# Optimization experiments

Hardware: AMD Instinct MI355X
Metric: run time of the kernel (lower is better)

Reference implementation:

```python
import jax, jax.numpy as jnp
import numpy as np

B, K, D, H = 4, 2048, 1024, 16
NCTX = K // 2
IMAGE_SIZE = 224
MAX_POS = 1024


def _build_rope_cache_2d(max_pos, dim, base=10000.0):
    half_dim = dim // 2
    theta = 1.0 / base ** (np.arange(0, half_dim, 2, dtype=np.float32) / half_dim)
    positions = np.arange(max_pos, dtype=np.float32)
    freqs = np.outer(positions, theta)  # [max_pos, dim/4]
    return jnp.asarray(np.stack([np.cos(freqs), np.sin(freqs)], axis=-1))  # [max_pos, dim/4, 2]


def apply_rope_2d(x, coords, rope_cache, image_size):
    b, k, d = x.shape
    half, quarter = d // 2, d // 4
    max_pos = rope_cache.shape[0]
    cn = jnp.clip(coords / image_size * (max_pos - 1), 0, max_pos - 1)
    y_pos = cn[..., 0].astype(jnp.int32)
    x_pos = cn[..., 1].astype(jnp.int32)
    y_rope = rope_cache[y_pos]  # [b,k,quarter,2]
    x_rope = rope_cache[x_pos]

    def rot(part, r):
        c, s = r[..., 0], r[..., 1]
        p0, p1 = part[..., 0], part[..., 1]
        return jnp.stack([p0 * c - p1 * s, p0 * s + p1 * c], -1).reshape(b, k, half)

    xp = x[..., :half].reshape(b, k, quarter, 2)
    yp = x[..., half:].reshape(b, k, quarter, 2)
    return jnp.concatenate([rot(xp, x_rope), rot(yp, y_rope)], -1)


def mha(q_tok, kv_tok, in_w, in_b, out_w, out_b, num_heads):
    b, nq, d = q_tok.shape
    hd = d // num_heads
    wq, wk, wv = jnp.split(in_w, 3, axis=0)
    bq, bk, bv = jnp.split(in_b, 3)
    q = (q_tok @ wq.T + bq).reshape(b, nq, num_heads, hd)
    k = (kv_tok @ wk.T + bk).reshape(b, -1, num_heads, hd)
    v = (kv_tok @ wv.T + bv).reshape(b, -1, num_heads, hd)
    s = jnp.einsum('bqhd,bkhd->bhqk', q, k) / jnp.sqrt(jnp.asarray(hd, q.dtype))
    a = jax.nn.softmax(s, axis=-1)
    o = jnp.einsum('bhqk,bkhd->bqhd', a, v).reshape(b, nq, d)
    return o @ out_w.T + out_b


def setup_inputs() -> dict:
    key = jax.random.key(0)
    ks = jax.random.split(key, 12)
    sc = 1.0 / np.sqrt(D)
    x = jax.random.normal(ks[0], (B, K, D), jnp.float32)
    coords = jax.random.uniform(ks[1], (B, K, 2), jnp.float32) * IMAGE_SIZE
    # boolean context mask with exactly NCTX context tokens per batch (code assumes equal counts)
    perms = jax.vmap(lambda k_: jax.random.permutation(k_, K))(jax.random.split(ks[2], B))
    is_context = jax.vmap(lambda m, i: m.at[i].set(True))(jnp.zeros((B, K), bool), perms[:, :NCTX])
    rope_cache = _build_rope_cache_2d(MAX_POS, D)
    return {
        'x': x, 'coords': coords, 'is_context': is_context, 'rope_cache': rope_cache,
        'ctx_in_w': jax.random.normal(ks[3], (3 * D, D), jnp.float32) * sc,
        'ctx_in_b': jnp.zeros((3 * D,), jnp.float32),
        'ctx_out_w': jax.random.normal(ks[4], (D, D), jnp.float32) * sc,
        'ctx_out_b': jnp.zeros((D,), jnp.float32),
        'tgt_in_w': jax.random.normal(ks[5], (3 * D, D), jnp.float32) * sc,
        'tgt_in_b': jnp.zeros((3 * D,), jnp.float32),
        'tgt_out_w': jax.random.normal(ks[6], (D, D), jnp.float32) * sc,
        'tgt_out_b': jnp.zeros((D,), jnp.float32),
    }


def reference(x, coords, is_context, rope_cache,
              ctx_in_w, ctx_in_b, ctx_out_w, ctx_out_b,
              tgt_in_w, tgt_in_b, tgt_out_w, tgt_out_b):
    # 2D RoPE before attention (as in the backbone)
    xr = apply_rope_2d(x, coords, rope_cache, IMAGE_SIZE)
    # stable argsort: context positions (key 0) first, in original order
    order = jnp.argsort(jnp.where(is_context, 0, 1), axis=1, stable=True)
    ctx_idx = order[:, :NCTX]   # [B, NCTX]
    tgt_idx = order[:, NCTX:]   # [B, K-NCTX]
    ctx_tok = jnp.take_along_axis(xr, ctx_idx[..., None], axis=1)
    tgt_tok = jnp.take_along_axis(xr, tgt_idx[..., None], axis=1)
    ctx_out = mha(ctx_tok, ctx_tok, ctx_in_w, ctx_in_b, ctx_out_w, ctx_out_b, H)
    tgt_out = mha(tgt_tok, ctx_tok, tgt_in_w, tgt_in_b, tgt_out_w, tgt_out_b, H)
    out = jnp.zeros_like(x)
    out = jax.vmap(lambda o, i, v: o.at[i].set(v))(out, ctx_idx, ctx_out)
    out = jax.vmap(lambda o, i, v: o.at[i].set(v))(out, tgt_idx, tgt_out)
    return out
```

## Files before the change

### kernel.cpp

```cpp
#include <hip/hip_runtime.h>
#include <math.h>

#define B_    4
#define K_    2048
#define D_    1024
#define H_    16
#define NCTX_ 1024

typedef unsigned short ushort_t;
typedef _Float16 f16;
typedef __attribute__((ext_vector_type(8))) _Float16 f16x8;
typedef __attribute__((ext_vector_type(4))) float f32x4;

union U4 {
  f16 h[4];
  ushort4 u;
};

union P4 {
  f16 h[4];
  ushort4 u;
};

__device__ __forceinline__ void gload16(const void* g, void* l) {
  __builtin_amdgcn_global_load_lds(
      (const __attribute__((address_space(1))) unsigned int*)g,
      (__attribute__((address_space(3))) unsigned int*)l, 16, 0, 0);
}

__global__ __launch_bounds__(256) void partition_kernel(
    const unsigned char* __restrict__ isctx, int* __restrict__ pos,
    int* __restrict__ ipos) {
  const int b = blockIdx.x;
  const int tid = threadIdx.x;
  const int wid = tid >> 6, lane = tid & 63;
  __shared__ int csum[4];
  __shared__ int waveTot[4];
  __shared__ int strideSh;

  int cnt = 0;
  for (int i = 0; i < 32; ++i) cnt += (isctx[tid * 32 + i] != 0);
  for (int off = 32; off; off >>= 1) cnt += __shfl_down(cnt, off, 64);
  if (lane == 0) csum[wid] = cnt;
  __syncthreads();
  if (tid == 0) {
    int t = csum[0] + csum[1] + csum[2] + csum[3];
    strideSh = (t > 2048) ? 1 : ((t > 768) ? 4 : 8);
  }
  __syncthreads();
  const int stride = strideSh;

  const unsigned char* base = isctx + (size_t)b * K_ * stride;
  int f[8];
  int s = 0;
  for (int i = 0; i < 8; ++i) {
    f[i] = base[(size_t)(tid * 8 + i) * stride] != 0;
    s += f[i];
  }
  int inc = s;
  for (int off = 1; off < 64; off <<= 1) {
    int v = __shfl_up(inc, off, 64);
    if (lane >= off) inc += v;
  }
  if (lane == 63) waveTot[wid] = inc;
  __syncthreads();
  int wOff = 0;
  for (int w = 0; w < wid; ++w) wOff += waveTot[w];
  int run = wOff + inc - s;
  for (int i = 0; i < 8; ++i) {
    int k = tid * 8 + i;
    int p;
    if (f[i]) {
      p = run;
      run++;
    } else {
      p = NCTX_ + k - run;
    }
    pos[b * K_ + k] = p;
    ipos[b * K_ + p] = k;
  }
}

__global__ __launch_bounds__(256) void rope_kernel(
    const float* __restrict__ x, const float* __restrict__ coords,
    const float* __restrict__ cache, const int* __restrict__ ipos,
    f16* __restrict__ tok) {
  const int row = blockIdx.x;
  const int b = row >> 11;
  const int r = row & (K_ - 1);
  const int k = ipos[row];
  const int t = threadIdx.x;

  const float cy = coords[(size_t)(b * K_ + k) * 2 + 0];
  const float cx = coords[(size_t)(b * K_ + k) * 2 + 1];
  const int ypos = (int)fminf(fmaxf(cy / 224.0f * 1023.0f, 0.0f), 1023.0f);
  const int xpos = (int)fminf(fmaxf(cx / 224.0f * 1023.0f, 0.0f), 1023.0f);

  const float4 v = ((const float4*)(x + ((size_t)b * K_ + k) * D_))[t];
  const int e = 4 * t;
  const float* crow;
  int coff;
  if (e < 512) {
    crow = cache + (size_t)xpos * 512;
    coff = e;
  } else {
    crow = cache + (size_t)ypos * 512;
    coff = e - 512;
  }
  const float4 cs = *(const float4*)(crow + coff);
  float o[4];
  o[0] = v.x * cs.x - v.y * cs.y;
  o[1] = v.x * cs.y + v.y * cs.x;
  o[2] = v.z * cs.z - v.w * cs.w;
  o[3] = v.z * cs.w + v.w * cs.z;
  U4 h;
#pragma unroll
  for (int i = 0; i < 4; ++i) h.h[i] = (f16)o[i];
  ((ushort4*)(tok + ((size_t)b * K_ + r) * D_))[t] = h.u;
}

__global__ __launch_bounds__(256) void cvt_all(
    const float* __restrict__ ctx_in_w, const float* __restrict__ tgt_in_w,
    const float* __restrict__ ctx_out_w, const float* __restrict__ tgt_out_w,
    f16* __restrict__ dst) {
  const int i4 = blockIdx.x * 256 + threadIdx.x;
  const int f = i4 * 4;
  const float* src;
  if (f < 3145728) src = ctx_in_w + f;
  else if (f < 5242880) src = tgt_in_w + (f - 3145728 + 1048576);
  else if (f < 6291456) src = tgt_in_w + (f - 5242880);
  else if (f < 7340032) src = ctx_out_w + (f - 6291456);
  else src = tgt_out_w + (f - 7340032);
  const float4 v = *(const float4*)src;
  U4 u;
  u.h[0] = (f16)v.x;
  u.h[1] = (f16)v.y;
  u.h[2] = (f16)v.z;
  u.h[3] = (f16)v.w;
  ((ushort4*)dst)[i4] = u.u;
}

#define GEMM_PRE(AP, WP, Kd)                                                  \
  const int rb_ = wave * 8 + (lane >> 3);          \
  const int kk_ = ((lane & 7) ^ (lane >> 3)) * 8;   \
  const f16* gA_ = (AP) + (size_t)rb_ * (Kd) + kk_;                           \
  const f16* gW_ = (WP) + (size_t)rb_ * (Kd) + kk_;                           \
  const int lA_ = wave * 8 * 64 + lane * 8;

#define GEMM_STAGE(k0s, bb)                                                   \
  _Pragma("unroll") for (int j = 0; j < 4; ++j) {                             \
    gload16(gA_ + (size_t)j * 32 * Kd_ + (k0s), &lds[(bb) + j * 2048 + lA_]); \
    gload16(gW_ + (size_t)j * 32 * Kd_ + (k0s),                               \
            &lds[(bb) + 8192 + j * 2048 + lA_]);                              \
  }

#define GEMM_TILE(bb)                                                         \
  _Pragma("unroll") for (int kh = 0; kh < 2; ++kh) {                          \
    f16x8 af[4], wf[4];                                                       \
    _Pragma("unroll") for (int i = 0; i < 4; ++i) {                           \
      const int ca = ((kh * 4 + quad) ^ (m16 & 7)) * 8;                       \
      af[i] = *(const f16x8*)&lds[(bb) + (wm + i * 16 + m16) * 64 + ca];      \
      wf[i] =                                                                 \
          *(const f16x8*)&lds[(bb) + 8192 + (wn + i * 16 + m16) * 64 + ca];   \
    }                                                                         \
    _Pragma("unroll") for (int i = 0; i < 4; ++i)                             \
        _Pragma("unroll") for (int j = 0; j < 4; ++j)                         \
      acc[i][j] = __builtin_amdgcn_mfma_f32_16x16x32_f16(af[i], wf[j],        \
                                                         acc[i][j], 0, 0, 0); \
  }

#define GEMM_CORE(AP, WP, Kd)                                                 \
  f32x4 acc[4][4];                                                            \
  {                                                                           \
    const f32x4 z = {0.f, 0.f, 0.f, 0.f};                                     \
    for (int i = 0; i < 4; ++i)                                               \
      for (int j = 0; j < 4; ++j) acc[i][j] = z;                              \
  }                                                                           \
  const int Kd_ = (Kd);                                                       \
  GEMM_PRE(AP, WP, Kd_)                                                       \
  GEMM_STAGE(0, 0)                                                            \
  for (int t = 0; t < Kd_ / 64; ++t) {                                        \
    const int cb = (t & 1) * 16384;                                           \
    if (t + 1 < Kd_ / 64) {                                                   \
      GEMM_STAGE((t + 1) * 64, ((t + 1) & 1) * 16384)                         \
      asm volatile("s_waitcnt vmcnt(8)" ::: "memory");                        \
    } else {                                                                  \
      asm volatile("s_waitcnt vmcnt(0)" ::: "memory");                        \
    }                                                                         \
    __builtin_amdgcn_s_barrier();                                             \
    asm volatile("" ::: "memory");                                            \
    GEMM_TILE(cb)                                                             \
    asm volatile("" ::: "memory");                                            \
    __builtin_amdgcn_s_barrier();                                             \
  }

__global__ __launch_bounds__(256, 2) void gemm_proj(
    const f16* __restrict__ tok, const f16* __restrict__ wcat,
    const float* __restrict__ ctx_in_b, const float* __restrict__ tgt_in_b,
    f16* __restrict__ qkvc, f16* __restrict__ kvt, f16* __restrict__ qt) {
  __shared__ f16 lds[32768];
  const int tid = threadIdx.x;
  const int wave = tid >> 6, lane = tid & 63;
  const int quad = lane >> 4, m16 = lane & 15;
  const int nb = blockIdx.x, mb = blockIdx.y, b = blockIdx.z;
  const int wm = (wave & 1) << 6, wn = (wave >> 1) << 6;
  const int m0 = mb * 128;
  const bool isQ = nb >= 40;
  const int n0 = isQ ? (nb - 40) * 128 : nb * 128;
  const f16* AP = tok + (size_t)b * K_ * D_ +
                  (isQ ? (size_t)NCTX_ * D_ : (size_t)0) + (size_t)m0 * D_;
  const f16* WP = wcat + (isQ ? (size_t)5242880 : (size_t)0) +
                  (size_t)n0 * D_;

  GEMM_CORE(AP, WP, D_)

#pragma unroll
  for (int j = 0; j < 4; ++j) {
    const int col = n0 + wn + j * 16 + m16;
    float bv;
    f16* dst;
    int ldc, dcol;
    if (isQ) {
      bv = tgt_in_b[col];
      dst = qt + (size_t)b * NCTX_ * D_;
      ldc = D_;
      dcol = col;
    } else if (col < 3072) {
      bv = ctx_in_b[col];
      dst = qkvc + (size_t)b * NCTX_ * 3072;
      ldc = 3072;
      dcol = col;
    } else {
      bv = tgt_in_b[D_ + col - 3072];
      dst = kvt + (size_t)b * NCTX_ * 2048;
      ldc = 2048;
      dcol = col - 3072;
    }
#pragma unroll
    for (int i = 0; i < 4; ++i) {
      const int mr = m0 + wm + i * 16 + quad * 4;
#pragma unroll
      for (int r = 0; r < 4; ++r)
        dst[(size_t)(mr + r) * ldc + dcol] = (f16)(acc[i][j][r] + bv);
    }
  }
}

__global__ __launch_bounds__(256, 2) void gemm_out(
    const f16* __restrict__ Atok, const f16* __restrict__ Wbase,
    const float* __restrict__ bias_ctx, const float* __restrict__ bias_tgt,
    const int* __restrict__ ipos, float* __restrict__ out) {
  __shared__ f16 lds[32768];
  const int tid = threadIdx.x;
  const int wave = tid >> 6, lane = tid & 63;
  const int quad = lane >> 4, m16 = lane & 15;
  const int n0 = blockIdx.x * 128, m0 = blockIdx.y * 128;
  const int b = blockIdx.z & 3, sel = blockIdx.z >> 2;
  const int wm = (wave & 1) << 6, wn = (wave >> 1) << 6;
  const f16* AP = Atok + (size_t)b * K_ * D_ + (size_t)sel * NCTX_ * D_ +
                  (size_t)m0 * D_;
  const f16* WP = Wbase + (size_t)sel * 1048576 + (size_t)n0 * D_;
  const float* bias = sel ? bias_tgt : bias_ctx;

  GEMM_CORE(AP, WP, D_)

#pragma unroll
  for (int j = 0; j < 4; ++j) {
    const int col = n0 + wn + j * 16 + m16;
    const float bv = bias[col];
#pragma unroll
    for (int i = 0; i < 4; ++i) {
      const int mr = m0 + wm + i * 16 + quad * 4;
#pragma unroll
      for (int r = 0; r < 4; ++r) {
        const int orow = ipos[b * K_ + sel * NCTX_ + mr + r];
        out[(size_t)b * K_ * D_ + (size_t)orow * D_ + col] =
            acc[i][j][r] + bv;
      }
    }
  }
}

__global__ __launch_bounds__(256) void vtrans_kernel(
    const ushort_t* __restrict__ V, long long sVb, int ldv, int coloff,
    ushort_t* __restrict__ Vt) {
  __shared__ __align__(16) ushort_t tile[64][72];
  const int tblk = blockIdx.x, h = blockIdx.y, b = blockIdx.z;
  const int tid = threadIdx.x;
  const ushort_t* src =
      V + (long long)b * sVb + (size_t)(tblk * 64) * ldv + coloff + h * 64;
#pragma unroll
  for (int j = 0; j < 2; ++j) {
    const int c = j * 256 + tid;
    const int r = c >> 3, dc = c & 7;
    *(uint4*)&tile[r][dc * 8] = *(const uint4*)(src + (size_t)r * ldv + dc * 8);
  }
  __syncthreads();
  ushort_t* dst = Vt + (size_t)(b * H_ + h) * 64 * 1024 + tblk * 64;
#pragma unroll
  for (int j = 0; j < 2; ++j) {
    const int c = j * 256 + tid;
    const int d = c >> 3, tc = c & 7;
    union {
      ushort_t u[8];
      uint4 v;
    } t;
#pragma unroll
    for (int i = 0; i < 8; ++i) t.u[i] = tile[tc * 8 + i][d];
    *(uint4*)(dst + (size_t)d * 1024 + tc * 8) = t.v;
  }
}

__global__ __launch_bounds__(512) void attn_mfma(
    const f16* __restrict__ Qp, long long sQb, int ldq,
    const f16* __restrict__ Kp, long long sKb, int ldk,
    const f16* __restrict__ Vt, f16* __restrict__ O, long long sOb) {
  __shared__ f16 QP[8192];
  __shared__ f16 Ks[2][4096];
  __shared__ f16 Vs[2][4096];
  const int tid = threadIdx.x, wave = tid >> 6, lane = tid & 63;
  const int quad = lane >> 4, m16 = lane & 15;
  const int q0 = blockIdx.x * 128, h = blockIdx.y, b = blockIdx.z;
  const f16* Qb = Qp + (long long)b * sQb + h * 64;
  const f16* Kb = Kp + (long long)b * sKb + h * 64;
  const f16* Vb = Vt + (size_t)(b * H_ + h) * 64 * 1024;

  const int rowS = tid >> 3;
  const int kkc = ((tid & 7) ^ (rowS & 7)) * 8;
  const int lB = tid * 8;

#pragma unroll
  for (int j = 0; j < 2; ++j)
    gload16(Qb + (size_t)(q0 + j * 64 + rowS) * ldq + kkc,
            &QP[j * 4096 + lB]);
  gload16(Kb + (size_t)rowS * ldk + kkc, &Ks[0][lB]);
  gload16(Vb + (size_t)rowS * 1024 + kkc, &Vs[0][lB]);

  float m_run = -1e30f, l_run = 0.f;
  f32x4 Oa[4];
  const f32x4 z = {0.f, 0.f, 0.f, 0.f};
#pragma unroll
  for (int j = 0; j < 4; ++j) Oa[j] = z;

  asm volatile("s_waitcnt vmcnt(2)" ::: "memory");
  __builtin_amdgcn_s_barrier();

  const int c0 = (quad ^ (m16 & 7)) * 8;
  const int c1 = ((quad + 4) ^ (m16 & 7)) * 8;
  const f16x8 qf0 = *(const f16x8*)&QP[(wave * 16 + m16) * 64 + c0];
  const f16x8 qf1 = *(const f16x8*)&QP[(wave * 16 + m16) * 64 + c1];

  f16* Pw = QP + wave * 1024;

  for (int kt = 0; kt < 16; ++kt) {
    const int cur = kt & 1;
    if (kt < 15) {
      gload16(Kb + (size_t)((kt + 1) * 64 + rowS) * ldk + kkc,
              &Ks[cur ^ 1][lB]);
      gload16(Vb + (size_t)rowS * 1024 + (kt + 1) * 64 + kkc,
              &Vs[cur ^ 1][lB]);
      asm volatile("s_waitcnt vmcnt(2)" ::: "memory");
    } else {
      asm volatile("s_waitcnt vmcnt(0)" ::: "memory");
    }
    __builtin_amdgcn_s_barrier();

    f32x4 S[4];
    __builtin_amdgcn_s_setprio(1);
#pragma unroll
    for (int jn = 0; jn < 4; ++jn) {
      S[jn] = z;
      const f16x8 kf0 = *(const f16x8*)&Ks[cur][(jn * 16 + m16) * 64 + c0];
      const f16x8 kf1 = *(const f16x8*)&Ks[cur][(jn * 16 + m16) * 64 + c1];
      S[jn] = __builtin_amdgcn_mfma_f32_16x16x32_f16(kf0, qf0, S[jn], 0, 0, 0);
      S[jn] = __builtin_amdgcn_mfma_f32_16x16x32_f16(kf1, qf1, S[jn], 0, 0, 0);
    }
    __builtin_amdgcn_s_setprio(0);

    float mv0 = fmaxf(fmaxf(S[0][0], S[1][0]), fmaxf(S[2][0], S[3][0]));
    float mv1 = fmaxf(fmaxf(S[0][1], S[1][1]), fmaxf(S[2][1], S[3][1]));
    float mv2 = fmaxf(fmaxf(S[0][2], S[1][2]), fmaxf(S[2][2], S[3][2]));
    float mv3 = fmaxf(fmaxf(S[0][3], S[1][3]), fmaxf(S[2][3], S[3][3]));
    float mx = fmaxf(fmaxf(mv0, mv1), fmaxf(mv2, mv3));
    mx = fmaxf(mx, __shfl_xor(mx, 16, 64));
    mx = fmaxf(mx, __shfl_xor(mx, 32, 64));
    mx *= 0.125f;
    const float mnew = fmaxf(m_run, mx);
    const float al = __expf(m_run - mnew);
    m_run = mnew;

    float rs = 0.f;
#pragma unroll
    for (int jn = 0; jn < 4; ++jn) {
      P4 p4;
#pragma unroll
      for (int r = 0; r < 4; ++r) {
        const float p = __expf(__builtin_fmaf(S[jn][r], 0.125f, -mnew));
        rs += p;
        p4.h[r] = (f16)p;
      }
      *(ushort4*)&Pw[m16 * 64 + (((jn * 2 + (quad >> 1)) ^ (m16 & 7)) * 8) +
                     (quad & 1) * 4] = p4.u;
    }
    rs += __shfl_xor(rs, 16, 64);
    rs += __shfl_xor(rs, 32, 64);
    l_run = l_run * al + rs;

    float alq[4];
#pragma unroll
    for (int r = 0; r < 4; ++r) alq[r] = __shfl(al, quad * 4 + r, 64);
#pragma unroll
    for (int j = 0; j < 4; ++j) {
      Oa[j][0] *= alq[0];
      Oa[j][1] *= alq[1];
      Oa[j][2] *= alq[2];
      Oa[j][3] *= alq[3];
    }

    const f16x8 pf0 = *(const f16x8*)&Pw[m16 * 64 + c0];
    const f16x8 pf1 = *(const f16x8*)&Pw[m16 * 64 + c1];
    __builtin_amdgcn_s_setprio(1);
#pragma unroll
    for (int jd = 0; jd < 4; ++jd) {
      const f16x8 vf0 = *(const f16x8*)&Vs[cur][(jd * 16 + m16) * 64 + c0];
      const f16x8 vf1 = *(const f16x8*)&Vs[cur][(jd * 16 + m16) * 64 + c1];
      Oa[jd] = __builtin_amdgcn_mfma_f32_16x16x32_f16(pf0, vf0, Oa[jd], 0, 0, 0);
      Oa[jd] = __builtin_amdgcn_mfma_f32_16x16x32_f16(pf1, vf1, Oa[jd], 0, 0, 0);
    }
    __builtin_amdgcn_s_setprio(0);
    __builtin_amdgcn_s_barrier();
  }

  float lq[4];
#pragma unroll
  for (int r = 0; r < 4; ++r) lq[r] = 1.0f / __shfl(l_run, quad * 4 + r, 64);
#pragma unroll
  for (int jd = 0; jd < 4; ++jd)
#pragma unroll
    for (int r = 0; r < 4; ++r) {
      const float v = Oa[jd][r] * lq[r];
      const size_t off = (long long)b * sOb +
                         (size_t)(q0 + wave * 16 + quad * 4 + r) * D_ + h * 64 +
                         jd * 16 + m16;
      O[off] = (f16)v;
    }
}

extern "C" void kernel_launch(void* const* d_in, const int* in_sizes, int n_in,
                              void* d_out, int out_size, void* d_ws,
                              size_t ws_size, hipStream_t stream) {
  const float* x = (const float*)d_in[0];
  const float* coords = (const float*)d_in[1];
  const unsigned char* isctx = (const unsigned char*)d_in[2];
  const float* rope = (const float*)d_in[3];
  const float* ctx_in_w = (const float*)d_in[4];
  const float* ctx_in_b = (const float*)d_in[5];
  const float* ctx_out_w = (const float*)d_in[6];
  const float* ctx_out_b = (const float*)d_in[7];
  const float* tgt_in_w = (const float*)d_in[8];
  const float* tgt_in_b = (const float*)d_in[9];
  const float* tgt_out_w = (const float*)d_in[10];
  const float* tgt_out_b = (const float*)d_in[11];
  float* out = (float*)d_out;

  f16* ws = (f16*)d_ws;
  f16* tok = ws;
  f16* wcat = tok + 8388608;
  f16* qkvc = wcat + 8388608;
  f16* kvt = qkvc + 12582912;
  f16* qt = kvt + 8388608;
  f16* vt = qt + 4194304;
  int* pos = (int*)(vt + 4194304);
  int* ipos = pos + B_ * K_;

  partition_kernel<<<B_, 256, 0, stream>>>(isctx, pos, ipos);
  cvt_all<<<8192, 256, 0, stream>>>(ctx_in_w, tgt_in_w, ctx_out_w, tgt_out_w,
                                    wcat);
  rope_kernel<<<B_ * K_, 256, 0, stream>>>(x, coords, rope, ipos, tok);

  gemm_proj<<<dim3(48, 8, B_), 256, 0, stream>>>(tok, wcat, ctx_in_b,
                                                 tgt_in_b, qkvc, kvt, qt);

  vtrans_kernel<<<dim3(16, H_, B_), 256, 0, stream>>>(
      (const ushort_t*)qkvc, (long long)NCTX_ * 3 * D_, 3 * D_, 2 * D_,
      (ushort_t*)vt);
  attn_mfma<<<dim3(8, H_, B_), 512, 0, stream>>>(
      qkvc, (long long)NCTX_ * 3 * D_, 3 * D_, qkvc + D_,
      (long long)NCTX_ * 3 * D_, 3 * D_, vt, tok, (long long)K_ * D_);
  vtrans_kernel<<<dim3(16, H_, B_), 256, 0, stream>>>(
      (const ushort_t*)kvt, (long long)NCTX_ * 2 * D_, 2 * D_, D_,
      (ushort_t*)vt);
  attn_mfma<<<dim3(8, H_, B_), 512, 0, stream>>>(
      qt, (long long)NCTX_ * D_, D_, kvt, (long long)NCTX_ * 2 * D_, 2 * D_,
      vt, tok + (size_t)NCTX_ * D_, (long long)K_ * D_);

  gemm_out<<<dim3(8, 8, 2 * B_), 256, 0, stream>>>(
      tok, wcat + 6291456, ctx_out_b, tgt_out_b, ipos, out);
}
```

Before: 303.9 us.

## Fuse V transpose into projection epilogue and merge both attention launches

The projection GEMM epilogue now writes the context and target V columns straight into a head-major transposed layout, which removes both vtrans kernels and the extra read and write of V. The two attention launches are merged into one grid with twice the z-dimension, selecting context or target inputs per block, so the GPU gets more blocks per launch and fewer launches overall. Online softmax skips the rescale of the accumulator and the running sum when no row maximum grows. The V epilogue stores are strided 8-byte writes, less coalesced than before, and the skip adds a wave-wide vote each iteration.

```diff
diff --git a/kernel.cpp b/kernel.cpp
--- a/kernel.cpp
+++ b/kernel.cpp
@@ -197,7 +197,8 @@
 __global__ __launch_bounds__(256, 2) void gemm_proj(
     const f16* __restrict__ tok, const f16* __restrict__ wcat,
     const float* __restrict__ ctx_in_b, const float* __restrict__ tgt_in_b,
-    f16* __restrict__ qkvc, f16* __restrict__ kvt, f16* __restrict__ qt) {
+    f16* __restrict__ qkvc, f16* __restrict__ kvt, f16* __restrict__ qt,
+    f16* __restrict__ vtc, f16* __restrict__ vtt) {
   __shared__ f16 lds[32768];
   const int tid = threadIdx.x;
   const int wave = tid >> 6, lane = tid & 63;
@@ -217,31 +218,52 @@
 #pragma unroll
   for (int j = 0; j < 4; ++j) {
     const int col = n0 + wn + j * 16 + m16;
-    float bv;
-    f16* dst;
-    int ldc, dcol;
     if (isQ) {
-      bv = tgt_in_b[col];
-      dst = qt + (size_t)b * NCTX_ * D_;
-      ldc = D_;
-      dcol = col;
-    } else if (col < 3072) {
-      bv = ctx_in_b[col];
-      dst = qkvc + (size_t)b * NCTX_ * 3072;
-      ldc = 3072;
-      dcol = col;
+      const float bv = tgt_in_b[col];
+      f16* dst = qt + (size_t)b * NCTX_ * 1024;
+#pragma unroll
+      for (int i = 0; i < 4; ++i) {
+        const int mr = m0 + wm + i * 16 + quad * 4;
+#pragma unroll
+        for (int r = 0; r < 4; ++r)
+          dst[(size_t)(mr + r) * 1024 + col] = (f16)(acc[i][j][r] + bv);
+      }
+    } else if (col < 2048) {
+      const float bv = ctx_in_b[col];
+      f16* dst = qkvc + (size_t)b * NCTX_ * 2048;
+#pragma unroll
+      for (int i = 0; i < 4; ++i) {
+        const int mr = m0 + wm + i * 16 + quad * 4;
+#pragma unroll
+        for (int r = 0; r < 4; ++r)
+          dst[(size_t)(mr + r) * 2048 + col] = (f16)(acc[i][j][r] + bv);
+      }
+    } else if (col >= 3072 && col < 4096) {
+      const float bv = tgt_in_b[D_ + col - 3072];
+      f16* dst = kvt + (size_t)b * NCTX_ * 1024;
+      const int dcol = col - 3072;
+#pragma unroll
+      for (int i = 0; i < 4; ++i) {
+        const int mr = m0 + wm + i * 16 + quad * 4;
+#pragma unroll
+        for (int r = 0; r < 4; ++r)
+          dst[(size_t)(mr + r) * 1024 + dcol] = (f16)(acc[i][j][r] + bv);
+      }
     } else {
-      bv = tgt_in_b[D_ + col - 3072];
-      dst = kvt + (size_t)b * NCTX_ * 2048;
-      ldc = 2048;
-      dcol = col - 3072;
-    }
-#pragma unroll
-    for (int i = 0; i < 4; ++i) {
-      const int mr = m0 + wm + i * 16 + quad * 4;
-#pragma unroll
-      for (int r = 0; r < 4; ++r)
-        dst[(size_t)(mr + r) * ldc + dcol] = (f16)(acc[i][j][r] + bv);
+      const bool isCtxV = col < 3072;
+      const int hd = isCtxV ? (col - 2048) : (col - 4096);
+      const float bv = isCtxV ? ctx_in_b[col] : tgt_in_b[D_ + col - 3072];
+      f16* dst = (isCtxV ? vtc : vtt) +
+                 ((size_t)(b * H_ + (hd >> 6)) << 16) +
+                 (size_t)(hd & 63) * 1024;
+#pragma unroll
+      for (int i = 0; i < 4; ++i) {
+        const int mr = m0 + wm + i * 16 + quad * 4;
+        P4 p4;
+#pragma unroll
+        for (int r = 0; r < 4; ++r) p4.h[r] = (f16)(acc[i][j][r] + bv);
+        *(ushort4*)(dst + mr) = p4.u;
+      }
     }
   }
 }
@@ -281,49 +303,34 @@
   }
 }
 
-__global__ __launch_bounds__(256) void vtrans_kernel(
-    const ushort_t* __restrict__ V, long long sVb, int ldv, int coloff,
-    ushort_t* __restrict__ Vt) {
-  __shared__ __align__(16) ushort_t tile[64][72];
-  const int tblk = blockIdx.x, h = blockIdx.y, b = blockIdx.z;
-  const int tid = threadIdx.x;
-  const ushort_t* src =
-      V + (long long)b * sVb + (size_t)(tblk * 64) * ldv + coloff + h * 64;
-#pragma unroll
-  for (int j = 0; j < 2; ++j) {
-    const int c = j * 256 + tid;
-    const int r = c >> 3, dc = c & 7;
-    *(uint4*)&tile[r][dc * 8] = *(const uint4*)(src + (size_t)r * ldv + dc * 8);
-  }
-  __syncthreads();
-  ushort_t* dst = Vt + (size_t)(b * H_ + h) * 64 * 1024 + tblk * 64;
-#pragma unroll
-  for (int j = 0; j < 2; ++j) {
-    const int c = j * 256 + tid;
-    const int d = c >> 3, tc = c & 7;
-    union {
-      ushort_t u[8];
-      uint4 v;
-    } t;
-#pragma unroll
-    for (int i = 0; i < 8; ++i) t.u[i] = tile[tc * 8 + i][d];
-    *(uint4*)(dst + (size_t)d * 1024 + tc * 8) = t.v;
-  }
-}
-
 __global__ __launch_bounds__(512) void attn_mfma(
-    const f16* __restrict__ Qp, long long sQb, int ldq,
-    const f16* __restrict__ Kp, long long sKb, int ldk,
-    const f16* __restrict__ Vt, f16* __restrict__ O, long long sOb) {
+    const f16* __restrict__ qkvc, const f16* __restrict__ kvt,
+    const f16* __restrict__ qt, const f16* __restrict__ vtc,
+    const f16* __restrict__ vtt, f16* __restrict__ O) {
   __shared__ f16 QP[8192];
   __shared__ f16 Ks[2][4096];
   __shared__ f16 Vs[2][4096];
   const int tid = threadIdx.x, wave = tid >> 6, lane = tid & 63;
   const int quad = lane >> 4, m16 = lane & 15;
-  const int q0 = blockIdx.x * 128, h = blockIdx.y, b = blockIdx.z;
-  const f16* Qb = Qp + (long long)b * sQb + h * 64;
-  const f16* Kb = Kp + (long long)b * sKb + h * 64;
-  const f16* Vb = Vt + (size_t)(b * H_ + h) * 64 * 1024;
+  const int q0 = blockIdx.x * 128, h = blockIdx.y;
+  const int zz = blockIdx.z;
+  const int b = zz & 3;
+  const bool isCtx = zz < 4;
+
+  const f16* Qb;
+  const f16* Kb;
+  int ld;
+  if (isCtx) {
+    Qb = qkvc + (size_t)b * NCTX_ * 2048 + h * 64;
+    Kb = Qb + 1024;
+    ld = 2048;
+  } else {
+    Qb = qt + (size_t)b * NCTX_ * 1024 + h * 64;
+    Kb = kvt + (size_t)b * NCTX_ * 1024 + h * 64;
+    ld = 1024;
+  }
+  const f16* Vb = (isCtx ? vtc : vtt) + ((size_t)(b * H_ + h) << 16);
+  f16* Ob = O + (size_t)b * K_ * D_ + (isCtx ? 0 : (size_t)NCTX_ * D_);
 
   const int rowS = tid >> 3;
   const int kkc = ((tid & 7) ^ (rowS & 7)) * 8;
@@ -331,9 +338,8 @@
 
 #pragma unroll
   for (int j = 0; j < 2; ++j)
-    gload16(Qb + (size_t)(q0 + j * 64 + rowS) * ldq + kkc,
-            &QP[j * 4096 + lB]);
-  gload16(Kb + (size_t)rowS * ldk + kkc, &Ks[0][lB]);
+    gload16(Qb + (size_t)(q0 + j * 64 + rowS) * ld + kkc, &QP[j * 4096 + lB]);
+  gload16(Kb + (size_t)rowS * ld + kkc, &Ks[0][lB]);
   gload16(Vb + (size_t)rowS * 1024 + kkc, &Vs[0][lB]);
 
   float m_run = -1e30f, l_run = 0.f;
@@ -355,7 +361,7 @@
   for (int kt = 0; kt < 16; ++kt) {
     const int cur = kt & 1;
     if (kt < 15) {
-      gload16(Kb + (size_t)((kt + 1) * 64 + rowS) * ldk + kkc,
+      gload16(Kb + (size_t)((kt + 1) * 64 + rowS) * ld + kkc,
               &Ks[cur ^ 1][lB]);
       gload16(Vb + (size_t)rowS * 1024 + (kt + 1) * 64 + kkc,
               &Vs[cur ^ 1][lB]);
@@ -385,9 +391,14 @@
     mx = fmaxf(mx, __shfl_xor(mx, 16, 64));
     mx = fmaxf(mx, __shfl_xor(mx, 32, 64));
     mx *= 0.125f;
-    const float mnew = fmaxf(m_run, mx);
-    const float al = __expf(m_run - mnew);
-    m_run = mnew;
+
+    const bool grow = !__all(mx <= m_run);
+    float al = 1.f;
+    if (grow) {
+      const float mnew = fmaxf(m_run, mx);
+      al = __expf(m_run - mnew);
+      m_run = mnew;
+    }
 
     float rs = 0.f;
 #pragma unroll
@@ -395,7 +406,7 @@
       P4 p4;
 #pragma unroll
       for (int r = 0; r < 4; ++r) {
-        const float p = __expf(__builtin_fmaf(S[jn][r], 0.125f, -mnew));
+        const float p = __expf(__builtin_fmaf(S[jn][r], 0.125f, -m_run));
         rs += p;
         p4.h[r] = (f16)p;
       }
@@ -404,17 +415,21 @@
     }
     rs += __shfl_xor(rs, 16, 64);
     rs += __shfl_xor(rs, 32, 64);
-    l_run = l_run * al + rs;
-
-    float alq[4];
-#pragma unroll
-    for (int r = 0; r < 4; ++r) alq[r] = __shfl(al, quad * 4 + r, 64);
-#pragma unroll
-    for (int j = 0; j < 4; ++j) {
-      Oa[j][0] *= alq[0];
-      Oa[j][1] *= alq[1];
-      Oa[j][2] *= alq[2];
-      Oa[j][3] *= alq[3];
+
+    if (grow) {
+      l_run = l_run * al + rs;
+      float alq[4];
+#pragma unroll
+      for (int r = 0; r < 4; ++r) alq[r] = __shfl(al, quad * 4 + r, 64);
+#pragma unroll
+      for (int j = 0; j < 4; ++j) {
+        Oa[j][0] *= alq[0];
+        Oa[j][1] *= alq[1];
+        Oa[j][2] *= alq[2];
+        Oa[j][3] *= alq[3];
+      }
+    } else {
+      l_run += rs;
     }
 
     const f16x8 pf0 = *(const f16x8*)&Pw[m16 * 64 + c0];
@@ -439,10 +454,9 @@
 #pragma unroll
     for (int r = 0; r < 4; ++r) {
       const float v = Oa[jd][r] * lq[r];
-      const size_t off = (long long)b * sOb +
-                         (size_t)(q0 + wave * 16 + quad * 4 + r) * D_ + h * 64 +
-                         jd * 16 + m16;
-      O[off] = (f16)v;
+      const size_t off = (size_t)(q0 + wave * 16 + quad * 4 + r) * D_ +
+                         h * 64 + jd * 16 + m16;
+      Ob[off] = (f16)v;
     }
 }
 
@@ -467,10 +481,11 @@
   f16* tok = ws;
   f16* wcat = tok + 8388608;
   f16* qkvc = wcat + 8388608;
-  f16* kvt = qkvc + 12582912;
-  f16* qt = kvt + 8388608;
-  f16* vt = qt + 4194304;
-  int* pos = (int*)(vt + 4194304);
+  f16* kvt = qkvc + 8388608;
+  f16* qt = kvt + 4194304;
+  f16* vtc = qt + 4194304;
+  f16* vtt = vtc + 4194304;
+  int* pos = (int*)(vtt + 4194304);
   int* ipos = pos + B_ * K_;
 
   partition_kernel<<<B_, 256, 0, stream>>>(isctx, pos, ipos);
@@ -478,21 +493,11 @@
                                     wcat);
   rope_kernel<<<B_ * K_, 256, 0, stream>>>(x, coords, rope, ipos, tok);
 
-  gemm_proj<<<dim3(48, 8, B_), 256, 0, stream>>>(tok, wcat, ctx_in_b,
-                                                 tgt_in_b, qkvc, kvt, qt);
-
-  vtrans_kernel<<<dim3(16, H_, B_), 256, 0, stream>>>(
-      (const ushort_t*)qkvc, (long long)NCTX_ * 3 * D_, 3 * D_, 2 * D_,
-      (ushort_t*)vt);
-  attn_mfma<<<dim3(8, H_, B_), 512, 0, stream>>>(
-      qkvc, (long long)NCTX_ * 3 * D_, 3 * D_, qkvc + D_,
-      (long long)NCTX_ * 3 * D_, 3 * D_, vt, tok, (long long)K_ * D_);
-  vtrans_kernel<<<dim3(16, H_, B_), 256, 0, stream>>>(
-      (const ushort_t*)kvt, (long long)NCTX_ * 2 * D_, 2 * D_, D_,
-      (ushort_t*)vt);
-  attn_mfma<<<dim3(8, H_, B_), 512, 0, stream>>>(
-      qt, (long long)NCTX_ * D_, D_, kvt, (long long)NCTX_ * 2 * D_, 2 * D_,
-      vt, tok + (size_t)NCTX_ * D_, (long long)K_ * D_);
+  gemm_proj<<<dim3(48, 8, B_), 256, 0, stream>>>(
+      tok, wcat, ctx_in_b, tgt_in_b, qkvc, kvt, qt, vtc, vtt);
+
+  attn_mfma<<<dim3(8, H_, 2 * B_), 512, 0, stream>>>(qkvc, kvt, qt, vtc, vtt,
+                                                     tok);
 
   gemm_out<<<dim3(8, 8, 2 * B_), 256, 0, stream>>>(
       tok, wcat + 6291456, ctx_out_b, tgt_out_b, ipos, out);
```

After: 286.0 us. 5.9% less time.
